# Kernel tuning notes

Measured on AMD Instinct MI355X. Metric: run time of the kernel, lower is better.

The kernel has to match this reference:

```python
import jax, jax.numpy as jnp
import numpy as np

B = 8; C = 128; EXP = 4; H = 112; W = 112; K = 3; PAD = 1; STRIDE = 1
IN_C = C * EXP  # 512
EPS = 1e-5


def setup_inputs() -> dict:
    key = jax.random.key(0)
    ks = jax.random.split(key, 24)
    f32 = jnp.float32

    def n(k, shape, s=0.05):
        return jax.random.normal(k, shape, f32) * s

    def bn_params(k):
        k1, k2, k3, k4 = jax.random.split(k, 4)
        g = 1.0 + 0.1 * jax.random.normal(k1, (), f32)  # placeholder, per-channel below
        return k1, k2, k3, k4

    inp = {}
    inp["x"] = jax.random.normal(ks[0], (B, IN_C, H, W), f32)
    # conv1: 1x1, 512 -> 128
    inp["w1"] = n(ks[1], (C, IN_C))
    inp["b1"] = n(ks[2], (C,))
    # bn1
    inp["g1"] = 1.0 + 0.1 * jax.random.normal(ks[3], (C,), f32)
    inp["be1"] = 0.1 * jax.random.normal(ks[4], (C,), f32)
    inp["m1"] = 0.1 * jax.random.normal(ks[5], (C,), f32)
    inp["v1"] = 1.0 + 0.1 * jax.random.uniform(ks[6], (C,), f32)
    # offset conv: 3x3, C -> 18 (small weights so sampling offsets stay modest)
    inp["woff"] = n(ks[7], (2 * K * K, C, K, K), 0.01)
    inp["boff"] = jnp.zeros((2 * K * K,), f32)
    # deformable conv weight: 3x3, C -> C
    inp["wd"] = n(ks[8], (C, C, K, K))
    inp["bd"] = n(ks[9], (C,))
    # bn2
    inp["g2"] = 1.0 + 0.1 * jax.random.normal(ks[10], (C,), f32)
    inp["be2"] = 0.1 * jax.random.normal(ks[11], (C,), f32)
    inp["m2"] = 0.1 * jax.random.normal(ks[12], (C,), f32)
    inp["v2"] = 1.0 + 0.1 * jax.random.uniform(ks[13], (C,), f32)
    # conv2: 1x1, 128 -> 512
    inp["w2"] = n(ks[14], (IN_C, C))
    inp["b2"] = n(ks[15], (IN_C,))
    # bn3
    inp["g3"] = 1.0 + 0.1 * jax.random.normal(ks[16], (IN_C,), f32)
    inp["be3"] = 0.1 * jax.random.normal(ks[17], (IN_C,), f32)
    inp["m3"] = 0.1 * jax.random.normal(ks[18], (IN_C,), f32)
    inp["v3"] = 1.0 + 0.1 * jax.random.uniform(ks[19], (IN_C,), f32)
    return inp


def conv1x1(x, w, b):
    return jnp.einsum("oc,bchw->bohw", w, x) + b[None, :, None, None]


def bn(x, g, be, m, v):
    inv = g / jnp.sqrt(v + EPS)
    return x * inv[None, :, None, None] + (be - m * inv)[None, :, None, None]


def conv3x3(x, w, b):
    out = jax.lax.conv_general_dilated(
        x, w, (STRIDE, STRIDE), ((PAD, PAD), (PAD, PAD)),
        dimension_numbers=("NCHW", "OIHW", "NCHW"))
    return out + b[None, :, None, None]


def deform_conv(x, offset, w, b):
    # x: [B, Cin, H, W]; offset: [B, 2*K*K, Ho, Wo] (y,x interleaved per kernel pt)
    Bn, Cin, Hh, Ww = x.shape
    Ho, Wo = offset.shape[2], offset.shape[3]
    P = Ho * Wo
    off = offset.reshape(Bn, K * K, 2, Ho, Wo)
    kk = jnp.arange(K * K)
    ky = (kk // K).astype(jnp.float32)  # 0..2
    kx = (kk % K).astype(jnp.float32)
    base_y = jnp.arange(Ho, dtype=jnp.float32) * STRIDE - PAD
    base_x = jnp.arange(Wo, dtype=jnp.float32) * STRIDE - PAD
    py = base_y[None, None, :, None] + ky[None, :, None, None] + off[:, :, 0]  # [B,9,Ho,Wo]
    px = base_x[None, None, None, :] + kx[None, :, None, None] + off[:, :, 1]
    y0 = jnp.floor(py); x0 = jnp.floor(px)
    dy = (py - y0).reshape(Bn, 1, -1)  # [B,1,9*P]
    dx = (px - x0).reshape(Bn, 1, -1)
    x_flat = x.reshape(Bn, Cin, Hh * Ww)

    def gather(yi, xi):
        valid = ((yi >= 0) & (yi <= Hh - 1) & (xi >= 0) & (xi <= Ww - 1))
        yc = jnp.clip(yi, 0, Hh - 1).astype(jnp.int32)
        xc = jnp.clip(xi, 0, Ww - 1).astype(jnp.int32)
        idx = (yc * Ww + xc).reshape(Bn, -1)  # [B, 9*P]
        g = jax.vmap(lambda xb, ib: xb[:, ib])(x_flat, idx)  # [B, Cin, 9*P]
        return g * valid.reshape(Bn, 1, -1).astype(x.dtype)

    v00 = gather(y0, x0)
    v01 = gather(y0, x0 + 1)
    v10 = gather(y0 + 1, x0)
    v11 = gather(y0 + 1, x0 + 1)
    cols = (v00 * (1 - dy) * (1 - dx) + v01 * (1 - dy) * dx
            + v10 * dy * (1 - dx) + v11 * dy * dx)  # [B, Cin, 9*P]
    cols = cols.reshape(Bn, Cin * K * K, P)
    out = jnp.einsum("oi,bip->bop", w.reshape(w.shape[0], -1), cols)
    out = out + b[None, :, None]
    return out.reshape(Bn, w.shape[0], Ho, Wo)


def reference(x, w1, b1, g1, be1, m1, v1, woff, boff, wd, bd,
              g2, be2, m2, v2, w2, b2, g3, be3, m3, v3):
    out = jax.nn.relu(bn(conv1x1(x, w1, b1), g1, be1, m1, v1))
    offset = conv3x3(out, woff, boff)
    out = deform_conv(out, offset, wd, bd)
    out = bn(out, g2, be2, m2, v2)
    out = bn(conv1x1(out, w2, b2), g3, be3, m3, v3)
    return jax.nn.relu(out + x)
```

## Files before the change

### kernel.cpp

```cpp
#include <hip/hip_runtime.h>
#include <hip/hip_bf16.h>


typedef __attribute__((ext_vector_type(8))) short short8;
typedef __attribute__((ext_vector_type(4))) float f32x4;

constexpr int Bn = 8;
constexpr int IC = 512;
constexpr int Cc = 128;
constexpr int Hh = 112;
constexpr int Ww = 112;
constexpr int Pp = Hh * Ww;
constexpr float EPSf = 1e-5f;

constexpr size_t OFS_OFFS  = 0;
constexpr size_t OFS_OUT2B = 2097152;
constexpr size_t OFS_W1B   = (size_t)Bn * Pp * IC / 2;
constexpr size_t OFS_W2B   = OFS_W1B + (size_t)Cc * IC / 2;
constexpr size_t OFS_WDB   = OFS_W2B + (size_t)IC * Cc / 2;
constexpr size_t OFS_WOFB  = OFS_WDB + (size_t)9 * Cc * Cc / 2;

__device__ __forceinline__ ushort f2bf(float f) {
  uint u = __float_as_uint(f);
  return (ushort)((u + 0x7fffu + ((u >> 16) & 1u)) >> 16);
}
__device__ __forceinline__ float bfLO(uint u) {
  return __uint_as_float(u << 16);
}
__device__ __forceinline__ float bfHI(uint u) {
  return __uint_as_float(u & 0xffff0000u);
}
__device__ __forceinline__ uint cvtpk(float a, float b) {
  __hip_bfloat162 h = __float22bfloat162_rn(make_float2(a, b));
  return *(uint*)&h;
}

__global__ __launch_bounds__(256) void prep_kernel(
    const float* __restrict__ w1, const float* __restrict__ w2,
    const float* __restrict__ wd, const float* __restrict__ woff,
    float* __restrict__ ws) {
  ushort* w1b  = (ushort*)(ws + OFS_W1B);
  ushort* w2b  = (ushort*)(ws + OFS_W2B);
  ushort* wdb  = (ushort*)(ws + OFS_WDB);
  ushort* wofb = (ushort*)(ws + OFS_WOFB);
  const int n1 = Cc * IC;
  const int n2 = IC * Cc;
  const int n3 = 9 * Cc * Cc;
  const int n4 = 9 * 32 * Cc;
  const int total = n1 + n2 + n3 + n4;
  for (int idx = blockIdx.x * blockDim.x + threadIdx.x; idx < total;
       idx += gridDim.x * blockDim.x) {
    if (idx < n1) {
      w1b[idx] = f2bf(w1[idx]);
    } else if (idx < n1 + n2) {
      int t = idx - n1;
      w2b[t] = f2bf(w2[t]);
    } else if (idx < n1 + n2 + n3) {
      int t = idx - n1 - n2;
      int k = t / (Cc * Cc), r = t % (Cc * Cc);
      int oc = r / Cc, ic = r % Cc;
      wdb[t] = f2bf(wd[(oc * Cc + ic) * 9 + k]);
    } else {
      int t = idx - n1 - n2 - n3;
      int k = t / (32 * Cc), r = t % (32 * Cc);
      int oc = r / Cc, ic = r % Cc;
      wofb[t] = (oc < 18) ? f2bf(woff[(oc * Cc + ic) * 9 + k]) : (ushort)0;
    }
  }
}

__global__ __launch_bounds__(256) void k1_fused_mfma(
    const float* __restrict__ x, const ushort* __restrict__ w1b,
    const float* __restrict__ b1, const float* __restrict__ g1,
    const float* __restrict__ be1, const float* __restrict__ m1,
    const float* __restrict__ v1, ushort* __restrict__ out1b) {
  __shared__ ushort At[64][136];

  const int tid = threadIdx.x;
  const int lane = tid & 63;
  const int wv = tid >> 6;
  const int lr = lane & 15, lg = lane >> 4;
  const int orig = blockIdx.x;
  const int bid = (orig & 7) * 196 + (orig >> 3);
  const int bi = bid / 196;
  const int p0 = (bid % 196) * 64;

  const int ic2 = (tid >> 2) * 2;
  const int pq = (tid & 3) * 4;

  const ushort* Bw = w1b + (size_t)(wv * 32) * IC;
  const float* xbase = x + (size_t)bi * IC * Pp + p0 + pq;

  f32x4 acc[4][2];
#pragma unroll
  for (int m = 0; m < 4; ++m) { acc[m][0] = (f32x4)0.f; acc[m][1] = (f32x4)0.f; }

  float4 pv0[4], pv1[4];
  {
    const float* r0 = xbase + (size_t)ic2 * Pp;
    const float* r1 = r0 + Pp;
#pragma unroll
    for (int i = 0; i < 4; ++i) {
      pv0[i] = *(const float4*)(r0 + 16 * i);
      pv1[i] = *(const float4*)(r1 + 16 * i);
    }
  }

#pragma unroll
  for (int ch = 0; ch < 4; ++ch) {
    const int c0 = ch * 128;
#pragma unroll
    for (int i = 0; i < 4; ++i) {
      int px = pq + 16 * i;
      *(uint*)&At[px + 0][ic2] = cvtpk(pv0[i].x, pv1[i].x);
      *(uint*)&At[px + 1][ic2] = cvtpk(pv0[i].y, pv1[i].y);
      *(uint*)&At[px + 2][ic2] = cvtpk(pv0[i].z, pv1[i].z);
      *(uint*)&At[px + 3][ic2] = cvtpk(pv0[i].w, pv1[i].w);
    }
    __syncthreads();

    if (ch < 3) {
      const float* r0 = xbase + (size_t)(c0 + 128 + ic2) * Pp;
      const float* r1 = r0 + Pp;
#pragma unroll
      for (int i = 0; i < 4; ++i) {
        pv0[i] = *(const float4*)(r0 + 16 * i);
        pv1[i] = *(const float4*)(r1 + 16 * i);
      }
    }

#pragma unroll
    for (int ks = 0; ks < 4; ++ks) {
      short8 b0 = *(const short8*)(Bw + (size_t)lr * IC + c0 + ks * 32 + 8 * lg);
      short8 b1v = *(const short8*)(Bw + (size_t)(16 + lr) * IC + c0 + ks * 32 + 8 * lg);
#pragma unroll
      for (int m = 0; m < 4; ++m) {
        short8 a = *(const short8*)&At[m * 16 + lr][ks * 32 + 8 * lg];
        acc[m][0] = __builtin_amdgcn_mfma_f32_16x16x32_bf16(a, b0, acc[m][0], 0, 0, 0);
        acc[m][1] = __builtin_amdgcn_mfma_f32_16x16x32_bf16(a, b1v, acc[m][1], 0, 0, 0);
      }
    }
    __syncthreads();
  }

#pragma unroll
  for (int n = 0; n < 2; ++n) {
    int oc = wv * 32 + n * 16 + lr;
    float inv = g1[oc] * rsqrtf(v1[oc] + EPSf);
    float sh = (b1[oc] - m1[oc]) * inv + be1[oc];
#pragma unroll
    for (int m = 0; m < 4; ++m) {
#pragma unroll
      for (int r = 0; r < 4; ++r) {
        int p = p0 + m * 16 + lg * 4 + r;
        out1b[((size_t)bi * Pp + p) * Cc + oc] =
            f2bf(fmaxf(acc[m][n][r] * inv + sh, 0.f));
      }
    }
  }
}

__global__ __launch_bounds__(256) void k2_offset_mfma(
    const ushort* __restrict__ out1b, const ushort* __restrict__ wofb,
    const float* __restrict__ boff, float* __restrict__ offs) {
  const int tid = threadIdx.x;
  const int lane = tid & 63;
  const int wv = tid >> 6;
  const int lr = lane & 15, lg = lane >> 4;
  const int orig = blockIdx.x;
  const int bid = (orig & 7) * 49 + (orig >> 3);
  const int bi = bid / 49;
  const int p0 = (bid % 49) * 256 + wv * 64;

  const ushort* src = out1b + (size_t)bi * Pp * Cc;

  int ohm[4], owm[4];
#pragma unroll
  for (int m = 0; m < 4; ++m) {
    int p = p0 + m * 16 + lr;
    ohm[m] = p / Ww;
    owm[m] = p - ohm[m] * Ww;
  }

  f32x4 acc[4][2];
#pragma unroll
  for (int m = 0; m < 4; ++m) { acc[m][0] = (f32x4)0.f; acc[m][1] = (f32x4)0.f; }

  for (int k = 0; k < 9; ++k) {
    const int kdy = k / 3 - 1, kdx = k % 3 - 1;
    const ushort* rp[4];
    bool val[4];
#pragma unroll
    for (int m = 0; m < 4; ++m) {
      int yy = ohm[m] + kdy, xx = owm[m] + kdx;
      val[m] = ((unsigned)yy < (unsigned)Hh) && ((unsigned)xx < (unsigned)Ww);
      int yc = min(max(yy, 0), Hh - 1), xc = min(max(xx, 0), Ww - 1);
      rp[m] = src + (size_t)(yc * Ww + xc) * Cc;
    }
#pragma unroll
    for (int ks = 0; ks < 4; ++ks) {
      short8 b0 = *(const short8*)(wofb + (size_t)(k * 32 + lr) * Cc + ks * 32 + 8 * lg);
      short8 b1v = *(const short8*)(wofb + (size_t)(k * 32 + 16 + lr) * Cc + ks * 32 + 8 * lg);
#pragma unroll
      for (int m = 0; m < 4; ++m) {
        short8 av = *(const short8*)(rp[m] + ks * 32 + 8 * lg);
        short8 a = val[m] ? av : (short8)0;
        acc[m][0] = __builtin_amdgcn_mfma_f32_16x16x32_bf16(a, b0, acc[m][0], 0, 0, 0);
        acc[m][1] = __builtin_amdgcn_mfma_f32_16x16x32_bf16(a, b1v, acc[m][1], 0, 0, 0);
      }
    }
  }

#pragma unroll
  for (int n = 0; n < 2; ++n) {
    int oc = n * 16 + lr;
    if (oc < 18) {
      float bo = boff[oc];
      float* orow = offs + ((size_t)bi * 18 + oc) * Pp;
#pragma unroll
      for (int m = 0; m < 4; ++m) {
        int p = p0 + m * 16 + lg * 4;
        float4 o;
        o.x = acc[m][n][0] + bo;
        o.y = acc[m][n][1] + bo;
        o.z = acc[m][n][2] + bo;
        o.w = acc[m][n][3] + bo;
        *(float4*)(orow + p) = o;
      }
    }
  }
}

__global__ __launch_bounds__(256) void k3_deform_mfma(
    const ushort* __restrict__ out1b, const float* __restrict__ offs,
    const ushort* __restrict__ wdb, const float* __restrict__ bd,
    const float* __restrict__ g2, const float* __restrict__ be2,
    const float* __restrict__ m2, const float* __restrict__ v2,
    ushort* __restrict__ out2b) {
  __shared__ ushort colsA[2][64][136];
  __shared__ float meta[9 * 64 * 8];

  const int tid = threadIdx.x;
  const int lane = tid & 63;
  const int wv = tid >> 6;
  const int lr = lane & 15, lg = lane >> 4;
  const int orig = blockIdx.x;
  const int bid = (orig & 7) * 196 + (orig >> 3);
  const int bi = bid / 196;
  const int p0 = (bid % 196) * 64;

  const ushort* src = out1b + (size_t)bi * Pp * Cc;
  const float* offb = offs + (size_t)bi * 18 * Pp;

  {
    const int p = p0 + lane;
    const int oh = p / Ww, ow = p - oh * Ww;
    for (int k = wv; k < 9; k += 4) {
      const int kdy = k / 3 - 1, kdx = k % 3 - 1;
      float py = (float)(oh + kdy) + offb[(size_t)(2 * k) * Pp + p];
      float pxf = (float)(ow + kdx) + offb[(size_t)(2 * k + 1) * Pp + p];
      float y0f = floorf(py), x0f = floorf(pxf);
      float dy = py - y0f, dx = pxf - x0f;
      int y0 = (int)y0f, x0 = (int)x0f;
      int y1 = y0 + 1, x1 = x0 + 1;
      float wy0 = (y0 >= 0 && y0 < Hh) ? 1.f - dy : 0.f;
      float wy1 = (y1 >= 0 && y1 < Hh) ? dy : 0.f;
      float wx0 = (x0 >= 0 && x0 < Ww) ? 1.f - dx : 0.f;
      float wx1 = (x1 >= 0 && x1 < Ww) ? dx : 0.f;
      int yc0 = min(max(y0, 0), Hh - 1), yc1 = min(max(y1, 0), Hh - 1);
      int xc0 = min(max(x0, 0), Ww - 1), xc1 = min(max(x1, 0), Ww - 1);
      float* mp = &meta[(k * 64 + lane) * 8];
      mp[0] = wy0 * wx0;
      mp[1] = wy0 * wx1;
      mp[2] = wy1 * wx0;
      mp[3] = wy1 * wx1;
      int* ip = (int*)(mp + 4);
      ip[0] = (yc0 * Ww + xc0) * (Cc * 2);
      ip[1] = (yc0 * Ww + xc1) * (Cc * 2);
      ip[2] = (yc1 * Ww + xc0) * (Cc * 2);
      ip[3] = (yc1 * Ww + xc1) * (Cc * 2);
    }
  }
  __syncthreads();

  f32x4 acc[4][2];
#pragma unroll
  for (int m = 0; m < 4; ++m) { acc[m][0] = (f32x4)0.f; acc[m][1] = (f32x4)0.f; }

  const int pxq = lane >> 4;
  const int l16 = lane & 15;
  const char* sb = (const char*)src + l16 * 16;

  uint4 gv[4][4];
  float4 gw[4];

#define BAR_LGKM asm volatile("s_waitcnt lgkmcnt(0)\ns_barrier" ::: "memory")

#define ISSUE(kk, t)                                                     \
  {                                                                      \
    const int px_ = wv * 16 + (t) * 4 + pxq;                             \
    const float* mp_ = &meta[((kk) * 64 + px_) * 8];                     \
    gw[t] = *(const float4*)mp_;                                         \
    int4 o4_ = *(const int4*)(mp_ + 4);                                  \
    gv[t][0] = *(const uint4*)(sb + o4_.x);                              \
    gv[t][1] = *(const uint4*)(sb + o4_.y);                              \
    gv[t][2] = *(const uint4*)(sb + o4_.z);                              \
    gv[t][3] = *(const uint4*)(sb + o4_.w);                              \
  }

#define COMMIT(buf, t)                                                   \
  {                                                                      \
    const int px_ = wv * 16 + (t) * 4 + pxq;                             \
    float4 w4_ = gw[t];                                                  \
    uint4 pk_;                                                           \
    uint* pkp_ = (uint*)&pk_;                                            \
    _Pragma("unroll")                                                    \
    for (int j = 0; j < 4; ++j) {                                        \
      uint a0_ = ((const uint*)&gv[t][0])[j];                            \
      uint a1_ = ((const uint*)&gv[t][1])[j];                            \
      uint a2_ = ((const uint*)&gv[t][2])[j];                            \
      uint a3_ = ((const uint*)&gv[t][3])[j];                            \
      float lo_ = w4_.x * bfLO(a0_) + w4_.y * bfLO(a1_)                  \
                + w4_.z * bfLO(a2_) + w4_.w * bfLO(a3_);                 \
      float hi_ = w4_.x * bfHI(a0_) + w4_.y * bfHI(a1_)                  \
                + w4_.z * bfHI(a2_) + w4_.w * bfHI(a3_);                 \
      pkp_[j] = cvtpk(lo_, hi_);                                         \
    }                                                                    \
    *(uint4*)&colsA[buf][px_][l16 * 8] = pk_;                            \
  }

  ISSUE(0, 0) ISSUE(0, 1) ISSUE(0, 2) ISSUE(0, 3)
  COMMIT(0, 0) COMMIT(0, 1) COMMIT(0, 2) COMMIT(0, 3)
  ISSUE(1, 0) ISSUE(1, 1) ISSUE(1, 2) ISSUE(1, 3)
  BAR_LGKM;

  for (int k = 0; k < 9; ++k) {
    const int cur = k & 1;
    const int nxt = cur ^ 1;
    const ushort* wk = wdb + (size_t)k * Cc * Cc + (size_t)(wv * 32) * Cc;

#pragma unroll
    for (int ks = 0; ks < 4; ++ks) {
      short8 b0 = *(const short8*)(wk + lr * Cc + ks * 32 + 8 * lg);
      short8 b1v = *(const short8*)(wk + (16 + lr) * Cc + ks * 32 + 8 * lg);
#pragma unroll
      for (int m = 0; m < 4; ++m) {
        short8 a = *(const short8*)&colsA[cur][m * 16 + lr][ks * 32 + 8 * lg];
        acc[m][0] = __builtin_amdgcn_mfma_f32_16x16x32_bf16(a, b0, acc[m][0], 0, 0, 0);
        acc[m][1] = __builtin_amdgcn_mfma_f32_16x16x32_bf16(a, b1v, acc[m][1], 0, 0, 0);
      }
    }

    if (k < 8) {
      COMMIT(nxt, 0)
      if (k < 7) { ISSUE(k + 2, 0) }
      COMMIT(nxt, 1)
      if (k < 7) { ISSUE(k + 2, 1) }
      COMMIT(nxt, 2)
      if (k < 7) { ISSUE(k + 2, 2) }
      COMMIT(nxt, 3)
      if (k < 7) { ISSUE(k + 2, 3) }
      BAR_LGKM;
    }
  }

#undef ISSUE
#undef COMMIT
#undef BAR_LGKM

#pragma unroll
  for (int n = 0; n < 2; ++n) {
    int oc = wv * 32 + n * 16 + lr;
    float inv = g2[oc] * rsqrtf(v2[oc] + EPSf);
    float sh = (bd[oc] - m2[oc]) * inv + be2[oc];
#pragma unroll
    for (int m = 0; m < 4; ++m) {
#pragma unroll
      for (int r = 0; r < 4; ++r) {
        int p = p0 + m * 16 + lg * 4 + r;
        out2b[((size_t)bi * Pp + p) * Cc + oc] = f2bf(acc[m][n][r] * inv + sh);
      }
    }
  }
}

__global__ __launch_bounds__(256, 2) void k4_mfma(
    const ushort* __restrict__ out2b, const ushort* __restrict__ w2b,
    const float* __restrict__ b2, const float* __restrict__ g3,
    const float* __restrict__ be3, const float* __restrict__ m3,
    const float* __restrict__ v3, const float* __restrict__ x,
    float* __restrict__ out) {
  __shared__ float obuf[2][16][260];

  const int tid = threadIdx.x;
  const int lane = tid & 63;
  const int wv = tid >> 6;
  const int lr = lane & 15, lg = lane >> 4;
  const int orig = blockIdx.x;
  const int bid = (orig & 7) * 392 + (orig >> 3);
  const int bi = bid / 392;
  const int r392 = bid % 392;
  const int oc_t = r392 / 49;
  const int pblk = (r392 % 49) * 256;
  const int p0 = pblk + wv * 64;
  const int ocb = oc_t * 64;

  const ushort* A = out2b + ((size_t)bi * Pp + p0) * Cc;
  const ushort* Bw = w2b + (size_t)ocb * Cc;

  float4 xv[4][4];
#pragma unroll
  for (int n = 0; n < 4; ++n)
#pragma unroll
    for (int it = 0; it < 4; ++it) {
      int oc = ocb + n * 16 + it * 4 + wv;
      xv[n][it] = *(const float4*)(x + ((size_t)bi * IC + oc) * Pp + pblk + lane * 4);
    }

  f32x4 acc[4][4];
#pragma unroll
  for (int m = 0; m < 4; ++m)
#pragma unroll
    for (int n = 0; n < 4; ++n) acc[m][n] = (f32x4)0.f;

#pragma unroll
  for (int ks = 0; ks < 4; ++ks) {
    short8 a[4];
#pragma unroll
    for (int m = 0; m < 4; ++m)
      a[m] = *(const short8*)(A + (size_t)(m * 16 + lr) * Cc + ks * 32 + 8 * lg);
#pragma unroll
    for (int n = 0; n < 4; ++n) {
      short8 b = *(const short8*)(Bw + (size_t)(n * 16 + lr) * Cc + ks * 32 + 8 * lg);
#pragma unroll
      for (int m = 0; m < 4; ++m)
        acc[m][n] = __builtin_amdgcn_mfma_f32_16x16x32_bf16(a[m], b, acc[m][n], 0, 0, 0);
    }
  }

#pragma unroll
  for (int n = 0; n < 4; ++n) {
    {
      int ocw = ocb + n * 16 + lr;
      float inv = g3[ocw] * rsqrtf(v3[ocw] + EPSf);
      float sh = (b2[ocw] - m3[ocw]) * inv + be3[ocw];
      float(*buf)[260] = obuf[n & 1];
#pragma unroll
      for (int m = 0; m < 4; ++m) {
        float4 o;
        o.x = acc[m][n][0] * inv + sh;
        o.y = acc[m][n][1] * inv + sh;
        o.z = acc[m][n][2] * inv + sh;
        o.w = acc[m][n][3] * inv + sh;
        *(float4*)&buf[lr][wv * 64 + m * 16 + lg * 4] = o;
      }
    }
    __syncthreads();
    {
      const float(*buf)[260] = obuf[n & 1];
#pragma unroll
      for (int it = 0; it < 4; ++it) {
        int r = it * 4 + wv;
        int oc = ocb + n * 16 + r;
        float4 v = *(const float4*)&buf[r][lane * 4];
        float4 xr = xv[n][it];
        float4 o;
        o.x = fmaxf(v.x + xr.x, 0.f);
        o.y = fmaxf(v.y + xr.y, 0.f);
        o.z = fmaxf(v.z + xr.z, 0.f);
        o.w = fmaxf(v.w + xr.w, 0.f);
        *(float4*)(out + ((size_t)bi * IC + oc) * Pp + pblk + lane * 4) = o;
      }
    }
  }
}

extern "C" void kernel_launch(void* const* d_in, const int* in_sizes, int n_in,
                              void* d_out, int out_size, void* d_ws, size_t ws_size,
                              hipStream_t stream) {
  const float* x    = (const float*)d_in[0];
  const float* w1   = (const float*)d_in[1];
  const float* b1   = (const float*)d_in[2];
  const float* g1   = (const float*)d_in[3];
  const float* be1  = (const float*)d_in[4];
  const float* m1   = (const float*)d_in[5];
  const float* v1   = (const float*)d_in[6];
  const float* woff = (const float*)d_in[7];
  const float* boff = (const float*)d_in[8];
  const float* wd   = (const float*)d_in[9];
  const float* bd   = (const float*)d_in[10];
  const float* g2   = (const float*)d_in[11];
  const float* be2  = (const float*)d_in[12];
  const float* m2   = (const float*)d_in[13];
  const float* v2   = (const float*)d_in[14];
  const float* w2   = (const float*)d_in[15];
  const float* b2   = (const float*)d_in[16];
  const float* g3   = (const float*)d_in[17];
  const float* be3  = (const float*)d_in[18];
  const float* m3   = (const float*)d_in[19];
  const float* v3   = (const float*)d_in[20];

  float* ws   = (float*)d_ws;
  float* out  = (float*)d_out;
  float*  offs  = ws + OFS_OFFS;
  ushort* out2b = (ushort*)(ws + OFS_OUT2B);
  ushort* w1b   = (ushort*)(ws + OFS_W1B);
  ushort* w2b   = (ushort*)(ws + OFS_W2B);
  ushort* wdb   = (ushort*)(ws + OFS_WDB);
  ushort* wofb  = (ushort*)(ws + OFS_WOFB);
  ushort* out1b = (ushort*)d_out;

  prep_kernel<<<512, 256, 0, stream>>>(w1, w2, wd, woff, ws);
  k1_fused_mfma<<<Bn * 196, 256, 0, stream>>>(x, w1b, b1, g1, be1, m1, v1, out1b);
  k2_offset_mfma<<<Bn * 49, 256, 0, stream>>>(out1b, wofb, boff, offs);
  k3_deform_mfma<<<Bn * 196, 256, 0, stream>>>(out1b, offs, wdb, bd,
                                               g2, be2, m2, v2, out2b);
  k4_mfma<<<Bn * 392, 256, 0, stream>>>(out2b, w2b, b2, g3, be3, m3, v3, x, out);
}
```

Before: 323.9 us.

## Restructure conv1 kernel with 128-pixel tiles, double-buffered LDS and staged stores

The first 1x1 conv kernel now gives each block 128 pixels by all 128 output channels, down from 64 pixels, and walks the 512 input channels in 16 chunks of 32. Both the x tile and the weight tile go through double-buffered, XOR-swizzled LDS with register prefetch two chunks ahead. The epilogue stages the bf16 results in LDS so global stores are 16-byte and coalesced rather than scattered 2-byte writes. This aims to cut redundant weight loads and store inefficiency, in exchange for more LDS (about 52 KB) and more accumulator registers per thread, which may lower occupancy.

```diff
diff --git a/kernel.cpp b/kernel.cpp
--- a/kernel.cpp
+++ b/kernel.cpp
@@ -74,89 +74,115 @@
     const float* __restrict__ b1, const float* __restrict__ g1,
     const float* __restrict__ be1, const float* __restrict__ m1,
     const float* __restrict__ v1, ushort* __restrict__ out1b) {
-  __shared__ ushort At[64][136];
+  __shared__ ushort smem[26624];
 
   const int tid = threadIdx.x;
   const int lane = tid & 63;
   const int wv = tid >> 6;
   const int lr = lane & 15, lg = lane >> 4;
   const int orig = blockIdx.x;
-  const int bid = (orig & 7) * 196 + (orig >> 3);
-  const int bi = bid / 196;
-  const int p0 = (bid % 196) * 64;
-
-  const int ic2 = (tid >> 2) * 2;
-  const int pq = (tid & 3) * 4;
-
-  const ushort* Bw = w1b + (size_t)(wv * 32) * IC;
-  const float* xbase = x + (size_t)bi * IC * Pp + p0 + pq;
-
-  f32x4 acc[4][2];
-#pragma unroll
-  for (int m = 0; m < 4; ++m) { acc[m][0] = (f32x4)0.f; acc[m][1] = (f32x4)0.f; }
-
-  float4 pv0[4], pv1[4];
-  {
-    const float* r0 = xbase + (size_t)ic2 * Pp;
-    const float* r1 = r0 + Pp;
-#pragma unroll
-    for (int i = 0; i < 4; ++i) {
-      pv0[i] = *(const float4*)(r0 + 16 * i);
-      pv1[i] = *(const float4*)(r1 + 16 * i);
-    }
-  }
-
-#pragma unroll
-  for (int ch = 0; ch < 4; ++ch) {
-    const int c0 = ch * 128;
-#pragma unroll
-    for (int i = 0; i < 4; ++i) {
-      int px = pq + 16 * i;
-      *(uint*)&At[px + 0][ic2] = cvtpk(pv0[i].x, pv1[i].x);
-      *(uint*)&At[px + 1][ic2] = cvtpk(pv0[i].y, pv1[i].y);
-      *(uint*)&At[px + 2][ic2] = cvtpk(pv0[i].z, pv1[i].z);
-      *(uint*)&At[px + 3][ic2] = cvtpk(pv0[i].w, pv1[i].w);
-    }
-    __syncthreads();
-
-    if (ch < 3) {
-      const float* r0 = xbase + (size_t)(c0 + 128 + ic2) * Pp;
-      const float* r1 = r0 + Pp;
-#pragma unroll
-      for (int i = 0; i < 4; ++i) {
-        pv0[i] = *(const float4*)(r0 + 16 * i);
-        pv1[i] = *(const float4*)(r1 + 16 * i);
-      }
-    }
-
-#pragma unroll
-    for (int ks = 0; ks < 4; ++ks) {
-      short8 b0 = *(const short8*)(Bw + (size_t)lr * IC + c0 + ks * 32 + 8 * lg);
-      short8 b1v = *(const short8*)(Bw + (size_t)(16 + lr) * IC + c0 + ks * 32 + 8 * lg);
-#pragma unroll
-      for (int m = 0; m < 4; ++m) {
-        short8 a = *(const short8*)&At[m * 16 + lr][ks * 32 + 8 * lg];
-        acc[m][0] = __builtin_amdgcn_mfma_f32_16x16x32_bf16(a, b0, acc[m][0], 0, 0, 0);
-        acc[m][1] = __builtin_amdgcn_mfma_f32_16x16x32_bf16(a, b1v, acc[m][1], 0, 0, 0);
-      }
-    }
-    __syncthreads();
-  }
-
-#pragma unroll
-  for (int n = 0; n < 2; ++n) {
-    int oc = wv * 32 + n * 16 + lr;
+  const int bid = (orig & 7) * 98 + (orig >> 3);
+  const int bi = bid / 98;
+  const int pblk = (bid % 98) * 128;
+
+  float xs[2][4][2][2];
+  short8 wsv[2][2];
+
+#define BAR_LGKM asm volatile("s_waitcnt lgkmcnt(0)\ns_barrier" ::: "memory")
+
+#define LOADX(c, s)                                                       \
+  {                                                                       \
+    const float* xb_ = x + ((size_t)bi * IC + (size_t)((c) * 32 + wv * 8)) * Pp \
+                         + pblk + lane;                                   \
+    _Pragma("unroll") for (int q = 0; q < 4; ++q) {                       \
+      _Pragma("unroll") for (int p = 0; p < 2; ++p) {                     \
+        xs[s][q][p][0] = xb_[(size_t)(2 * q + p) * Pp];                   \
+        xs[s][q][p][1] = xb_[(size_t)(2 * q + p) * Pp + 64];              \
+      }                                                                   \
+    }                                                                     \
+  }
+
+#define LOADW(c, s)                                                       \
+  {                                                                       \
+    const ushort* wb_ = w1b + (size_t)(wv * 32 + (lane >> 2)) * IC        \
+                            + (c) * 32 + (lane & 3) * 8;                  \
+    wsv[s][0] = *(const short8*)(wb_);                                    \
+    wsv[s][1] = *(const short8*)(wb_ + (size_t)16 * IC);                  \
+  }
+
+#define WRITE(c, s)                                                       \
+  {                                                                       \
+    char* atb_ = (char*)smem + ((c) & 1) * 16384;                         \
+    _Pragma("unroll") for (int e = 0; e < 2; ++e) {                       \
+      const int px_ = lane + 64 * e;                                      \
+      uint4 pk_;                                                          \
+      uint* pp_ = (uint*)&pk_;                                            \
+      _Pragma("unroll") for (int q = 0; q < 4; ++q)                       \
+        pp_[q] = cvtpk(xs[s][q][0][e], xs[s][q][1][e]);                   \
+      *(uint4*)(atb_ + px_ * 128 + ((wv ^ (px_ & 7)) << 4)) = pk_;        \
+    }                                                                     \
+    ushort* wlb_ = smem + 16384 + ((c) & 1) * 5120;                       \
+    *(short8*)(wlb_ + (wv * 32 + (lane >> 2)) * 40 + (lane & 3) * 8) = wsv[s][0]; \
+    *(short8*)(wlb_ + (wv * 32 + 16 + (lane >> 2)) * 40 + (lane & 3) * 8) = wsv[s][1]; \
+  }
+
+  f32x4 acc[2][8];
+#pragma unroll
+  for (int m = 0; m < 2; ++m)
+#pragma unroll
+    for (int n = 0; n < 8; ++n) acc[m][n] = (f32x4)0.f;
+
+  LOADX(0, 0) LOADW(0, 0)
+  LOADX(1, 1) LOADW(1, 1)
+
+#pragma unroll
+  for (int c = 0; c < 16; ++c) {
+    WRITE(c, c & 1);
+    BAR_LGKM;
+    if (c + 2 < 16) { LOADX(c + 2, c & 1) LOADW(c + 2, c & 1) }
+
+    {
+      const char* atb = (const char*)smem + (c & 1) * 16384;
+      const ushort* wlb = smem + 16384 + (c & 1) * 5120;
+      const int sw = (lg ^ (lr & 7)) << 4;
+      short8 a0 = *(const short8*)(atb + (wv * 32 + lr) * 128 + sw);
+      short8 a1 = *(const short8*)(atb + (wv * 32 + 16 + lr) * 128 + sw);
+#pragma unroll
+      for (int n = 0; n < 8; ++n) {
+        short8 b = *(const short8*)(wlb + (n * 16 + lr) * 40 + lg * 8);
+        acc[0][n] = __builtin_amdgcn_mfma_f32_16x16x32_bf16(a0, b, acc[0][n], 0, 0, 0);
+        acc[1][n] = __builtin_amdgcn_mfma_f32_16x16x32_bf16(a1, b, acc[1][n], 0, 0, 0);
+      }
+    }
+  }
+
+#undef LOADX
+#undef LOADW
+#undef WRITE
+#undef BAR_LGKM
+
+  __syncthreads();
+
+  ushort(*Ab)[136] = (ushort(*)[136])smem;
+#pragma unroll
+  for (int n = 0; n < 8; ++n) {
+    int oc = n * 16 + lr;
     float inv = g1[oc] * rsqrtf(v1[oc] + EPSf);
     float sh = (b1[oc] - m1[oc]) * inv + be1[oc];
 #pragma unroll
-    for (int m = 0; m < 4; ++m) {
+    for (int m = 0; m < 2; ++m) {
 #pragma unroll
       for (int r = 0; r < 4; ++r) {
-        int p = p0 + m * 16 + lg * 4 + r;
-        out1b[((size_t)bi * Pp + p) * Cc + oc] =
-            f2bf(fmaxf(acc[m][n][r] * inv + sh, 0.f));
-      }
-    }
+        int pl = wv * 32 + m * 16 + lg * 4 + r;
+        Ab[pl][oc] = f2bf(fmaxf(acc[m][n][r] * inv + sh, 0.f));
+      }
+    }
+  }
+#pragma unroll
+  for (int j = 0; j < 8; ++j) {
+    int pl = wv * 32 + j * 4 + (lane >> 4);
+    uint4 v = *(const uint4*)&Ab[pl][(lane & 15) * 8];
+    *(uint4*)(out1b + ((size_t)bi * Pp + pblk + pl) * Cc + (lane & 15) * 8) = v;
   }
 }
 
@@ -511,7 +537,7 @@
   ushort* out1b = (ushort*)d_out;
 
   prep_kernel<<<512, 256, 0, stream>>>(w1, w2, wd, woff, ws);
-  k1_fused_mfma<<<Bn * 196, 256, 0, stream>>>(x, w1b, b1, g1, be1, m1, v1, out1b);
+  k1_fused_mfma<<<Bn * 98, 256, 0, stream>>>(x, w1b, b1, g1, be1, m1, v1, out1b);
   k2_offset_mfma<<<Bn * 49, 256, 0, stream>>>(out1b, wofb, boff, offs);
   k3_deform_mfma<<<Bn * 196, 256, 0, stream>>>(out1b, offs, wdb, bd,
                                                g2, be2, m2, v2, out2b);
```

Result: faster. 313.8 us (-3.1%).
